# Kernel tuning notes

Hardware: AMD Instinct MI355X
Metric: run time of the kernel (lower is better)

The kernel has to match this reference:

```python
import jax, jax.numpy as jnp
import numpy as np

B, N, D, H = 8, 2048, 128, 8
HD = D // H  # head_depth = 16
CLIP = 10.0
INF = 1e10
THETA = 10000.0
SCALE_BASE = 512.0
LOGIT_SCALE = float(np.log(400.0) / np.log(50.0) / np.sqrt(HD))


def _rotate_half(x):
    # interleaved pairs: (x1, x2) -> (-x2, x1)
    x1 = x[..., ::2]
    x2 = x[..., 1::2]
    return jnp.stack((-x2, x1), axis=-1).reshape(x.shape)


def _rope_xpos(n, hd):
    # rotary_embedding_torch RotaryEmbedding(dim=hd, use_xpos=True)
    inv_freq = 1.0 / (THETA ** (jnp.arange(0, hd, 2, dtype=jnp.float32) / hd))  # (hd/2,)
    t = jnp.arange(n, dtype=jnp.float32)
    freqs = t[:, None] * inv_freq[None, :]          # (n, hd/2)
    freqs = jnp.repeat(freqs, 2, axis=-1)           # (n, hd) interleaved dup
    sc = (jnp.arange(0, hd, 2, dtype=jnp.float32) + 0.4 * hd) / (1.4 * hd)  # (hd/2,)
    power = (t - (n // 2)) / SCALE_BASE             # centered positions
    scale = sc[None, :] ** power[:, None]           # (n, hd/2)
    scale = jnp.repeat(scale, 2, axis=-1)           # (n, hd)
    return freqs, scale


def setup_inputs() -> dict:
    key = jax.random.key(0)
    ks = jax.random.split(key, 7)
    stdv_qkv = 1.0 / np.sqrt(HD)
    stdv_out = 1.0 / np.sqrt(D)
    q = jax.random.normal(ks[0], (B, N, D), dtype=jnp.float32)
    k = jax.random.normal(ks[1], (B, N, D), dtype=jnp.float32)
    v = jax.random.normal(ks[2], (B, N, D), dtype=jnp.float32)
    Wq = jax.random.uniform(ks[3], (D, D), minval=-stdv_qkv, maxval=stdv_qkv, dtype=jnp.float32)
    Wk = jax.random.uniform(ks[4], (D, D), minval=-stdv_qkv, maxval=stdv_qkv, dtype=jnp.float32)
    Wv = jax.random.uniform(ks[5], (D, D), minval=-stdv_qkv, maxval=stdv_qkv, dtype=jnp.float32)
    Wout = jax.random.uniform(ks[6], (D, D), minval=-stdv_out, maxval=stdv_out, dtype=jnp.float32)
    mask = jnp.zeros((B, N, 1), dtype=bool)
    return {"q": q, "k": k, "v": v, "Wq": Wq, "Wk": Wk, "Wv": Wv, "Wout": Wout, "mask": mask}


def reference(q, k, v, Wq, Wk, Wv, Wout, mask):
    def split_heads(t, W):
        # torch Linear (bias=False): t @ W.T, then (B,N,H,HD) -> (B,H,N,HD)
        return (t @ W.T).reshape(B, N, H, HD).transpose(0, 2, 1, 3)

    Qh = split_heads(q, Wq)
    Kh = split_heads(k, Wk)
    Vh = split_heads(v, Wv)

    freqs, scale = _rope_xpos(N, HD)  # (N, HD) each, broadcast over (B,H,N,HD)
    cos, sin = jnp.cos(freqs), jnp.sin(freqs)
    Qr = Qh * (cos * scale) + _rotate_half(Qh) * (sin * scale)
    inv_scale = 1.0 / scale
    Kr = Kh * (cos * inv_scale) + _rotate_half(Kh) * (sin * inv_scale)

    logits = jnp.einsum('bhqd,bhkd->bhqk', Qr, Kr) * LOGIT_SCALE
    logits = CLIP * jnp.tanh(logits)
    # mask: (B,N,1) bool, True -> masked; broadcast to (B,1,1,N)
    logits = jnp.where(mask[:, None, None, :, 0], -INF, logits)
    probs = jax.nn.softmax(logits, axis=-1)
    out = jnp.einsum('bhqk,bhkd->bhqd', probs, Vh)
    out = out.transpose(0, 2, 1, 3).reshape(B, N, D)
    return out @ Wout.T
```

## Files before the change

kernel.cpp:

```cpp
#include <hip/hip_runtime.h>
#include <math.h>

#define BB 8
#define NN 2048
#define DD 128
#define HH 8

typedef _Float16 v4h __attribute__((ext_vector_type(4)));
typedef _Float16 v8h __attribute__((ext_vector_type(8)));
typedef float    v4f __attribute__((ext_vector_type(4)));
typedef float    v16f __attribute__((ext_vector_type(16)));

__device__ __forceinline__ v4f zero4() { v4f z = {0.f, 0.f, 0.f, 0.f}; return z; }
__device__ __forceinline__ v16f zero16() {
    v16f z;
    #pragma unroll
    for (int i = 0; i < 16; ++i) z[i] = 0.f;
    return z;
}

__device__ __forceinline__ v4f mfma16(v4h a, v4h b, v4f c) {
    return __builtin_amdgcn_mfma_f32_16x16x16f16(a, b, c, 0, 0, 0);
}
__device__ __forceinline__ v16f mfma32(v8h a, v8h b, v16f c) {
    return __builtin_amdgcn_mfma_f32_32x32x16_f16(a, b, c, 0, 0, 0);
}

__device__ __forceinline__ float fexp2(float x) {
#if __has_builtin(__builtin_amdgcn_exp2f)
    return __builtin_amdgcn_exp2f(x);
#else
    return __expf(x * 0.69314718055994531f);
#endif
}

#define QSCALE 1.10478088f
#define C1F 14.426950408889634f
#define C2F 28.853900817779268f

__global__ __launch_bounds__(256) void prep_kernel(
    const float* __restrict__ Wq, const float* __restrict__ Wk,
    const float* __restrict__ Wv, const float* __restrict__ Wo,
    _Float16* __restrict__ WH, _Float16* __restrict__ WoH,
    float* __restrict__ rtab)
{
    int tid = blockIdx.x * 256 + threadIdx.x;
    int m = tid >> 14, i = tid & 16383;
    const float* src = (m == 0) ? Wq : (m == 1) ? Wk : (m == 2) ? Wv : Wo;
    float wv = src[i];
    if (m < 3) WH[m * 16384 + i] = (_Float16)wv;
    else       WoH[i] = (_Float16)wv;

    if (tid < NN * 16) {
        int t = tid >> 4, hd = tid & 15, j = hd >> 1;
        const float invf_tab[8] = {1.f, 0.31622776601683794f, 0.1f, 0.031622776601683791f,
                                   0.01f, 0.0031622776601683794f, 0.001f, 0.00031622776601683794f};
        float freq = (float)t * invf_tab[j];
        float c = cosf(freq), s = sinf(freq);
        float scf = ((float)(2 * j) + 6.4f) / 22.4f;
        float pw  = ((float)t - 1024.0f) / 512.0f;
        float scl = exp2f(pw * log2f(scf));
        rtab[0 * NN * 16 + tid] = c * scl * QSCALE;
        rtab[1 * NN * 16 + tid] = s * scl * QSCALE;
        float is = 1.0f / scl;
        rtab[2 * NN * 16 + tid] = c * is;
        rtab[3 * NN * 16 + tid] = s * is;
    }
}

__global__ __launch_bounds__(256) void proj_rope_kernel(
    const float* __restrict__ q, const float* __restrict__ k, const float* __restrict__ v,
    const _Float16* __restrict__ WH, const float* __restrict__ rtab,
    _Float16* __restrict__ Qr, _Float16* __restrict__ Kr, _Float16* __restrict__ VT)
{
    __shared__ __align__(16) _Float16 xb[64][136];
    const int tid = threadIdx.x;
    const int m  = blockIdx.y;
    const int r0 = blockIdx.x * 64;
    const int b  = r0 >> 11;
    const int n0 = r0 & 2047;

    const float* s = ((m == 0) ? q : (m == 1) ? k : v) + (size_t)r0 * 128;
    #pragma unroll
    for (int i = 0; i < 8; ++i) {
        int u = tid + i * 256;
        int row = u >> 5, c4 = (u & 31) * 4;
        v4f f = *(const v4f*)(s + row * 128 + c4);
        v4h hv; hv[0]=(_Float16)f[0]; hv[1]=(_Float16)f[1]; hv[2]=(_Float16)f[2]; hv[3]=(_Float16)f[3];
        *(v4h*)&xb[row][c4] = hv;
    }
    __syncthreads();

    const int w = tid >> 6, lane = tid & 63;
    const int l16 = lane & 15, quad = lane >> 4;

    v4h xf[8];
    #pragma unroll
    for (int kt = 0; kt < 8; ++kt)
        xf[kt] = *(const v4h*)&xb[w * 16 + l16][kt * 16 + quad * 4];
    const _Float16* Wm = WH + m * 16384;
    v4f acc[8];
    #pragma unroll
    for (int ct = 0; ct < 8; ++ct) acc[ct] = zero4();
    #pragma unroll
    for (int kt = 0; kt < 8; ++kt) {
        #pragma unroll
        for (int ct = 0; ct < 8; ++ct) {
            v4h wf = *(const v4h*)(Wm + (ct * 16 + l16) * 128 + kt * 16 + quad * 4);
            if (m < 2) acc[ct] = mfma16(wf, xf[kt], acc[ct]);
            else       acc[ct] = mfma16(xf[kt], wf, acc[ct]);
        }
    }
    if (m < 2) {
        const float* tc = rtab + (m == 0 ? 0 : 2 * NN * 16);
        const float* ts = tc + NN * 16;
        const int n = n0 + w * 16 + l16;
        _Float16* dst = (m == 0 ? Qr : Kr);
        #pragma unroll
        for (int ct = 0; ct < 8; ++ct) {
            v4f cs = *(const v4f*)(tc + n * 16 + quad * 4);
            v4f sn = *(const v4f*)(ts + n * 16 + quad * 4);
            v4f a = acc[ct];
            v4f rot; rot[0] = -a[1]; rot[1] = a[0]; rot[2] = -a[3]; rot[3] = a[2];
            v4h o;
            #pragma unroll
            for (int r = 0; r < 4; ++r) o[r] = (_Float16)(a[r] * cs[r] + rot[r] * sn[r]);
            *(v4h*)(dst + ((size_t)(b * 8 + ct) * NN + n) * 16 + quad * 4) = o;
        }
    } else {
        #pragma unroll
        for (int ct = 0; ct < 8; ++ct) {
            v4f a = acc[ct];
            v4h o;
            #pragma unroll
            for (int r = 0; r < 4; ++r) o[r] = (_Float16)a[r];
            *(v4h*)(VT + ((size_t)(b * 8 + ct) * 16 + l16) * NN + n0 + w * 16 + quad * 4) = o;
        }
    }
}

__global__ __launch_bounds__(256, 6) void attn_kernel(
    const _Float16* __restrict__ Qr, const _Float16* __restrict__ Kr,
    const _Float16* __restrict__ VT, const unsigned char* __restrict__ mask,
    _Float16* __restrict__ Obuf)
{
    __shared__ __align__(16) char smem[15360];
    _Float16* Kt = (_Float16*)smem;
    _Float16* Ve = (_Float16*)(smem + 6144);
    float*    av = (float*)(smem + 14848);

    const int tid = threadIdx.x;
    const int bh = blockIdx.x >> 4;
    const int qt = blockIdx.x & 15;
    const int b = bh >> 3, h = bh & 7;
    const int q0 = qt * 128;
    const int w = tid >> 6, lane = tid & 63;
    const int l32 = lane & 31, hi = lane >> 5;

    const int qrow = q0 + w * 32 + l32;
    v8h qf = *(const v8h*)(Qr + ((size_t)bh * NN + qrow) * 16 + hi * 8);

    {
        v8h one8;
        #pragma unroll
        for (int i = 0; i < 8; ++i) one8[i] = (_Float16)1.f;
        *(v8h*)(Ve + (16 + (tid >> 4)) * 136 + (tid & 15) * 8) = one8;
    }

    v16f acc = zero16();

    const int krow = tid >> 1, kpar = tid & 1;
    const int vhd = tid >> 4, vg = tid & 15;

    for (int k0 = 0; k0 < NN; k0 += 128) {
        __syncthreads();
        v8h kv = *(const v8h*)(Kr + ((size_t)bh * NN + k0 + krow) * 16 + kpar * 8);
        *(v8h*)(Kt + krow * 24 + kpar * 8) = kv;
        v8h vv = *(const v8h*)(VT + ((size_t)bh * 16 + vhd) * NN + k0 + vg * 8);
        {
            _Float16* vb = Ve + vhd * 136 + (vg >> 1) * 16 + (vg & 1) * 4;
            v4h lo4, hi4;
            lo4[0]=vv[0]; lo4[1]=vv[1]; lo4[2]=vv[2]; lo4[3]=vv[3];
            hi4[0]=vv[4]; hi4[1]=vv[5]; hi4[2]=vv[6]; hi4[3]=vv[7];
            *(v4h*)(vb)     = lo4;
            *(v4h*)(vb + 8) = hi4;
        }
        if (tid < 128) av[tid] = mask[b * NN + k0 + tid] ? -1e30f : C1F;
        __syncthreads();

        #pragma unroll
        for (int kc = 0; kc < 4; ++kc) {
            v8h kf = *(const v8h*)(Kt + (kc * 32 + l32) * 24 + hi * 8);
            v16f sv = mfma32(kf, qf, zero16());

            v4f ad[4];
            #pragma unroll
            for (int g = 0; g < 4; ++g)
                ad[g] = *(const v4f*)(av + kc * 32 + g * 8 + hi * 4);

            float p[16];
            #pragma unroll
            for (int r = 0; r < 16; ++r) {
                float u  = fexp2(sv[r]);
                float rc = __builtin_amdgcn_rcpf(u + 1.f);
                p[r] = fexp2(__builtin_fmaf(rc, -C2F, ad[r >> 2][r & 3]));
            }

            #pragma unroll
            for (int c2 = 0; c2 < 2; ++c2) {
                v8h pa;
                #pragma unroll
                for (int j = 0; j < 8; ++j) pa[j] = (_Float16)p[c2 * 8 + j];
                v8h vf = *(const v8h*)(Ve + l32 * 136 + (kc * 2 + c2) * 16 + hi * 8);
                acc = mfma32(pa, vf, acc);
            }
        }
    }

    float rs[16];
    #pragma unroll
    for (int r = 0; r < 16; ++r) rs[r] = __shfl_xor(acc[r], 16, 64);

    __syncthreads();
    _Float16* myOt = (_Float16*)smem + w * 768;
    if (!(lane & 16)) {
        int j = lane & 15;
        #pragma unroll
        for (int r = 0; r < 16; ++r) {
            int qr = (r & 3) + 8 * (r >> 2) + 4 * hi;
            myOt[qr * 24 + j] = (_Float16)(acc[r] * __builtin_amdgcn_rcpf(rs[r]));
        }
    }
    asm volatile("s_waitcnt lgkmcnt(0)" ::: "memory");
    v8h ov = *(const v8h*)(myOt + (lane >> 1) * 24 + (lane & 1) * 8);
    *(v8h*)(Obuf + ((size_t)(b * NN + q0 + w * 32 + (lane >> 1)) * 128) + h * 16 + (lane & 1) * 8) = ov;
}

__global__ __launch_bounds__(256) void outproj_kernel(
    const _Float16* __restrict__ Obuf, const _Float16* __restrict__ WoH,
    float* __restrict__ out)
{
    __shared__ __align__(16) _Float16 ob[64][136];
    const int tid = threadIdx.x;
    const int r0 = blockIdx.x * 64;
    const int ct0 = blockIdx.y * 2;
    #pragma unroll
    for (int i = 0; i < 8; ++i) {
        int u = tid + i * 256;
        int row = u >> 5, c4 = (u & 31) * 4;
        *(v4h*)&ob[row][c4] = *(const v4h*)(Obuf + (size_t)(r0 + row) * 128 + c4);
    }
    __syncthreads();
    const int w = tid >> 6, lane = tid & 63;
    const int l16 = lane & 15, quad = lane >> 4;
    v4h af[8];
    #pragma unroll
    for (int kt = 0; kt < 8; ++kt)
        af[kt] = *(const v4h*)&ob[w * 16 + l16][kt * 16 + quad * 4];
    v4f acc[2];
    #pragma unroll
    for (int c = 0; c < 2; ++c) acc[c] = zero4();
    #pragma unroll
    for (int kt = 0; kt < 8; ++kt)
        #pragma unroll
        for (int c = 0; c < 2; ++c) {
            v4h wf = *(const v4h*)(WoH + ((ct0 + c) * 16 + l16) * 128 + kt * 16 + quad * 4);
            acc[c] = mfma16(af[kt], wf, acc[c]);
        }
    #pragma unroll
    for (int c = 0; c < 2; ++c)
        #pragma unroll
        for (int r = 0; r < 4; ++r)
            out[(size_t)(r0 + w * 16 + quad * 4 + r) * 128 + (ct0 + c) * 16 + l16] = acc[c][r];
}

extern "C" void kernel_launch(void* const* d_in, const int* in_sizes, int n_in,
                              void* d_out, int out_size, void* d_ws, size_t ws_size,
                              hipStream_t stream)
{
    const float* q  = (const float*)d_in[0];
    const float* k  = (const float*)d_in[1];
    const float* v  = (const float*)d_in[2];
    const float* Wq = (const float*)d_in[3];
    const float* Wk = (const float*)d_in[4];
    const float* Wv = (const float*)d_in[5];
    const float* Wo = (const float*)d_in[6];
    const unsigned char* mask = (const unsigned char*)d_in[7];
    float* out = (float*)d_out;

    char* ws = (char*)d_ws;
    _Float16* WH   = (_Float16*)(ws);
    _Float16* WoH  = (_Float16*)(ws + 98304);
    float*    rtab = (float*)(ws + 131072);
    _Float16* Qr   = (_Float16*)(ws + 655360);
    _Float16* Kr   = (_Float16*)(ws + 4849664);
    _Float16* VTd  = (_Float16*)(ws + 9043968);
    _Float16* Obuf = (_Float16*)(ws + 13238272);

    prep_kernel<<<256, 256, 0, stream>>>(Wq, Wk, Wv, Wo, WH, WoH, rtab);
    proj_rope_kernel<<<dim3(256, 3), 256, 0, stream>>>(q, k, v, WH, rtab, Qr, Kr, VTd);
    attn_kernel<<<1024, 256, 0, stream>>>(Qr, Kr, VTd, mask, Obuf);
    outproj_kernel<<<dim3(256, 4), 256, 0, stream>>>(Obuf, WoH, out);
}
```

Before: 196.0 us.

## Split attention key range across two warp groups per block and merge partials

The attention block grows from 256 to 512 threads. Each 256-thread half processes one half of the key sequence for the same 128 queries, with its own shared K/V staging buffer. The halves' unnormalized accumulators and row sums are combined through shared memory before normalization and write-out. This doubles the waves per block to improve latency hiding and the parallelism inside each block, at the cost of an extra reduction step, more shared memory, and a tighter register budget under launch_bounds(512,8).

```diff
diff --git a/kernel.cpp b/kernel.cpp
--- a/kernel.cpp
+++ b/kernel.cpp
@@ -139,40 +139,47 @@
     }
 }
 
-__global__ __launch_bounds__(256, 6) void attn_kernel(
+__global__ __launch_bounds__(512, 8) void attn_kernel(
     const _Float16* __restrict__ Qr, const _Float16* __restrict__ Kr,
     const _Float16* __restrict__ VT, const unsigned char* __restrict__ mask,
     _Float16* __restrict__ Obuf)
 {
-    __shared__ __align__(16) char smem[15360];
-    _Float16* Kt = (_Float16*)smem;
-    _Float16* Ve = (_Float16*)(smem + 6144);
-    float*    av = (float*)(smem + 14848);
+    __shared__ __align__(16) char smem[30720];
 
     const int tid = threadIdx.x;
+    const int g  = tid >> 8;
+    const int ts = tid & 255;
+    char* halfb = smem + g * 15360;
+    _Float16* Kt = (_Float16*)halfb;
+    _Float16* Ve = (_Float16*)(halfb + 6144);
+    float*    av = (float*)(halfb + 14848);
+
     const int bh = blockIdx.x >> 4;
     const int qt = blockIdx.x & 15;
     const int b = bh >> 3, h = bh & 7;
     const int q0 = qt * 128;
     const int w = tid >> 6, lane = tid & 63;
+    const int wq = w & 3;
     const int l32 = lane & 31, hi = lane >> 5;
 
-    const int qrow = q0 + w * 32 + l32;
+    const int qrow = q0 + wq * 32 + l32;
     v8h qf = *(const v8h*)(Qr + ((size_t)bh * NN + qrow) * 16 + hi * 8);
 
     {
         v8h one8;
         #pragma unroll
         for (int i = 0; i < 8; ++i) one8[i] = (_Float16)1.f;
-        *(v8h*)(Ve + (16 + (tid >> 4)) * 136 + (tid & 15) * 8) = one8;
+        *(v8h*)(Ve + (16 + (ts >> 4)) * 136 + (ts & 15) * 8) = one8;
     }
 
     v16f acc = zero16();
 
-    const int krow = tid >> 1, kpar = tid & 1;
-    const int vhd = tid >> 4, vg = tid & 15;
-
-    for (int k0 = 0; k0 < NN; k0 += 128) {
+    const int krow = ts >> 1, kpar = ts & 1;
+    const int vhd = ts >> 4, vg = ts & 15;
+    const int kbase = g * 1024;
+
+    for (int it = 0; it < 8; ++it) {
+        const int k0 = kbase + it * 128;
         __syncthreads();
         v8h kv = *(const v8h*)(Kr + ((size_t)bh * NN + k0 + krow) * 16 + kpar * 8);
         *(v8h*)(Kt + krow * 24 + kpar * 8) = kv;
@@ -185,7 +192,7 @@
             *(v4h*)(vb)     = lo4;
             *(v4h*)(vb + 8) = hi4;
         }
-        if (tid < 128) av[tid] = mask[b * NN + k0 + tid] ? -1e30f : C1F;
+        if (ts < 128) av[ts] = mask[b * NN + k0 + ts] ? -1e30f : C1F;
         __syncthreads();
 
         #pragma unroll
@@ -195,8 +202,8 @@
 
             v4f ad[4];
             #pragma unroll
-            for (int g = 0; g < 4; ++g)
-                ad[g] = *(const v4f*)(av + kc * 32 + g * 8 + hi * 4);
+            for (int gg = 0; gg < 4; ++gg)
+                ad[gg] = *(const v4f*)(av + kc * 32 + gg * 8 + hi * 4);
 
             float p[16];
             #pragma unroll
@@ -222,18 +229,35 @@
     for (int r = 0; r < 16; ++r) rs[r] = __shfl_xor(acc[r], 16, 64);
 
     __syncthreads();
-    _Float16* myOt = (_Float16*)smem + w * 768;
-    if (!(lane & 16)) {
+    float* pair = (float*)smem;
+    if (g == 1 && !(lane & 16)) {
         int j = lane & 15;
+        float* pb = pair + wq * 544;
         #pragma unroll
         for (int r = 0; r < 16; ++r) {
             int qr = (r & 3) + 8 * (r >> 2) + 4 * hi;
-            myOt[qr * 24 + j] = (_Float16)(acc[r] * __builtin_amdgcn_rcpf(rs[r]));
-        }
-    }
-    asm volatile("s_waitcnt lgkmcnt(0)" ::: "memory");
-    v8h ov = *(const v8h*)(myOt + (lane >> 1) * 24 + (lane & 1) * 8);
-    *(v8h*)(Obuf + ((size_t)(b * NN + q0 + w * 32 + (lane >> 1)) * 128) + h * 16 + (lane & 1) * 8) = ov;
+            pb[qr * 17 + j] = acc[r];
+            if (j == 0) pb[qr * 17 + 16] = rs[r];
+        }
+    }
+    __syncthreads();
+    if (g == 0) {
+        _Float16* myOt = (_Float16*)(smem + 8704) + wq * 768;
+        if (!(lane & 16)) {
+            int j = lane & 15;
+            const float* pb = pair + wq * 544;
+            #pragma unroll
+            for (int r = 0; r < 16; ++r) {
+                int qr = (r & 3) + 8 * (r >> 2) + 4 * hi;
+                float tot = acc[r] + pb[qr * 17 + j];
+                float rst = rs[r]  + pb[qr * 17 + 16];
+                myOt[qr * 24 + j] = (_Float16)(tot * __builtin_amdgcn_rcpf(rst));
+            }
+        }
+        asm volatile("s_waitcnt lgkmcnt(0)" ::: "memory");
+        v8h ov = *(const v8h*)(myOt + (lane >> 1) * 24 + (lane & 1) * 8);
+        *(v8h*)(Obuf + ((size_t)(b * NN + q0 + wq * 32 + (lane >> 1)) * 128) + h * 16 + (lane & 1) * 8) = ov;
+    }
 }
 
 __global__ __launch_bounds__(256) void outproj_kernel(
@@ -299,6 +323,6 @@
 
     prep_kernel<<<256, 256, 0, stream>>>(Wq, Wk, Wv, Wo, WH, WoH, rtab);
     proj_rope_kernel<<<dim3(256, 3), 256, 0, stream>>>(q, k, v, WH, rtab, Qr, Kr, VTd);
-    attn_kernel<<<1024, 256, 0, stream>>>(Qr, Kr, VTd, mask, Obuf);
+    attn_kernel<<<1024, 512, 0, stream>>>(Qr, Kr, VTd, mask, Obuf);
     outproj_kernel<<<dim3(256, 4), 256, 0, stream>>>(Obuf, WoH, out);
 }
```

Measured after the change: 197.2 us. No clear change (+0.6%).
